# Performance work log

Measured on AMD Instinct MI355X. Metric: run time of the kernel, lower is better.

## Reference

```python
import jax, jax.numpy as jnp
import numpy as np

N_NODES = 65536
N_EDGES = 1048576


def gcn_conv(x, edge_index, edge_weight, W, b):
    """PyG GCNConv: h = D^{-1/2}(A+I)D^{-1/2} x W + b, scatter to target (edge_index[1])."""
    n = x.shape[0]
    row, col = edge_index[0], edge_index[1]
    loop = jnp.arange(n)
    row_f = jnp.concatenate([row, loop])
    col_f = jnp.concatenate([col, loop])
    w_f = jnp.concatenate([edge_weight, jnp.ones((n,), dtype=x.dtype)])
    deg = jax.ops.segment_sum(w_f, col_f, num_segments=n)
    dis = jnp.where(deg > 0, jax.lax.rsqrt(jnp.where(deg > 0, deg, 1.0)), 0.0)
    norm = dis[row_f] * w_f * dis[col_f]  # [E+N]
    h = x @ W  # [N, out]
    msg = h[row_f] * norm[:, None]  # gather + scale
    out = jax.ops.segment_sum(msg, col_f, num_segments=n)
    return out + b


def setup_inputs() -> dict:
    key = jax.random.key(0)
    ks = jax.random.split(key, 8)
    x = jax.random.normal(ks[0], (N_NODES, 128), dtype=jnp.float32)
    edge_index = jax.random.randint(ks[1], (2, N_EDGES), 0, N_NODES, dtype=jnp.int64)
    edge_weight = jax.random.uniform(ks[2], (N_EDGES,), dtype=jnp.float32)
    W1 = jax.random.normal(ks[3], (128, 256), dtype=jnp.float32) * (128 ** -0.5)
    b1 = jnp.zeros((256,), dtype=jnp.float32)
    W2 = jax.random.normal(ks[4], (256, 128), dtype=jnp.float32) * (256 ** -0.5)
    b2 = jnp.zeros((128,), dtype=jnp.float32)
    W3 = jax.random.normal(ks[5], (128, 64), dtype=jnp.float32) * (128 ** -0.5)
    b3 = jnp.zeros((64,), dtype=jnp.float32)
    return {"x": x, "edge_index": edge_index, "edge_weight": edge_weight,
            "num_graphs": 64, "W1": W1, "b1": b1, "W2": W2, "b2": b2, "W3": W3, "b3": b3}


def reference(x, edge_index, edge_weight, num_graphs, W1, b1, W2, b2, W3, b3):
    h = jax.nn.relu(gcn_conv(x, edge_index, edge_weight, W1, b1))
    h = jax.nn.relu(gcn_conv(h, edge_index, edge_weight, W2, b2))
    h = gcn_conv(h, edge_index, edge_weight, W3, b3)  # [N, 64]
    g = h.reshape(num_graphs, -1, 64)
    pad = jnp.zeros((g.shape[0], 1, g.shape[2]), dtype=g.dtype)
    return jnp.concatenate([g, pad], axis=1)  # [num_graphs, nodes_per_graph+1, 64]
```

## Files before the change

### kernel.cpp

```cpp
#include <hip/hip_runtime.h>
#include <cstdint>

#define TPB 256

typedef __attribute__((ext_vector_type(8))) short bf16x8;
typedef __attribute__((ext_vector_type(4))) float f32x4;

__device__ inline unsigned short f2bf(float f) {
  unsigned u = __float_as_uint(f);
  u += 0x7fffu + ((u >> 16) & 1u);
  return (unsigned short)(u >> 16);
}
__device__ inline float bf2f(unsigned short h) {
  return __uint_as_float(((unsigned)h) << 16);
}

__device__ inline void gload_lds16(const void* g, void* l) {
  __builtin_amdgcn_global_load_lds(
      (const __attribute__((address_space(1))) unsigned int*)g,
      (__attribute__((address_space(3))) unsigned int*)l, 16, 0, 0);
}

__device__ inline void acc_bf8(float* acc, int4 raw, float nv) {
  acc[0] += nv * __uint_as_float(((unsigned)raw.x) << 16);
  acc[1] += nv * __uint_as_float(((unsigned)raw.x) & 0xffff0000u);
  acc[2] += nv * __uint_as_float(((unsigned)raw.y) << 16);
  acc[3] += nv * __uint_as_float(((unsigned)raw.y) & 0xffff0000u);
  acc[4] += nv * __uint_as_float(((unsigned)raw.z) << 16);
  acc[5] += nv * __uint_as_float(((unsigned)raw.z) & 0xffff0000u);
  acc[6] += nv * __uint_as_float(((unsigned)raw.w) << 16);
  acc[7] += nv * __uint_as_float(((unsigned)raw.w) & 0xffff0000u);
}


__global__ void k_count_deg(const int* __restrict__ col, const float* __restrict__ w,
                            unsigned long long* __restrict__ pk, int E) {
  int e = blockIdx.x * blockDim.x + threadIdx.x;
  if (e >= E) return;
  int c = col[e];
  unsigned long long inc =
      (1ULL << 40) + (unsigned long long)(unsigned int)(w[e] * 4294967296.0f);
  atomicAdd(&pk[c], inc);
}

__global__ void k_decode(const unsigned long long* __restrict__ pk, float* __restrict__ dis,
                         int* __restrict__ cnt, int n) {
  int i = blockIdx.x * blockDim.x + threadIdx.x;
  if (i >= n) return;
  unsigned long long v = pk[i];
  cnt[i] = (int)(v >> 40);
  float degs = (float)(v & 0xFFFFFFFFFFULL) * 2.3283064365386963e-10f;
  dis[i] = rsqrtf(1.0f + degs);
}


__global__ void k_reduceA(const int* __restrict__ cnt, int* __restrict__ bsum) {
  __shared__ int s[256];
  int t = threadIdx.x;
  s[t] = cnt[blockIdx.x * 256 + t];
  __syncthreads();
  for (int st = 128; st > 0; st >>= 1) {
    if (t < st) s[t] += s[t + st];
    __syncthreads();
  }
  if (t == 0) bsum[blockIdx.x] = s[0];
}

__global__ void k_scanB(const int* __restrict__ bsum, int* __restrict__ boff) {
  __shared__ int s[256];
  int t = threadIdx.x;
  int v = bsum[t];
  s[t] = v;
  __syncthreads();
  for (int st = 1; st < 256; st <<= 1) {
    int a = (t >= st) ? s[t - st] : 0;
    __syncthreads();
    s[t] += a;
    __syncthreads();
  }
  boff[t] = s[t] - v;
}

__global__ void k_scanC(const int* __restrict__ cnt, const int* __restrict__ boff,
                        int* __restrict__ ptr, int* __restrict__ cur, int n) {
  __shared__ int s[256];
  int t = threadIdx.x;
  int i = blockIdx.x * 256 + t;
  int v = cnt[i];
  s[t] = v;
  __syncthreads();
  for (int st = 1; st < 256; st <<= 1) {
    int a = (t >= st) ? s[t - st] : 0;
    __syncthreads();
    s[t] += a;
    __syncthreads();
  }
  int excl = boff[blockIdx.x] + s[t] - v;
  ptr[i] = excl;
  cur[i] = excl;
  if (i == n - 1) ptr[n] = excl + v;
}


__global__ void k_scatter_norm(const int* __restrict__ row, const int* __restrict__ col,
                               const float* __restrict__ w, const float* __restrict__ dis,
                               int* __restrict__ cur, int2* __restrict__ edat, int E) {
  int e = blockIdx.x * blockDim.x + threadIdx.x;
  if (e >= E) return;
  int c = col[e];
  int r = row[e];
  float nv = dis[r] * w[e] * dis[c];
  int p = atomicAdd(&cur[c], 1);
  edat[p] = make_int2(r, __float_as_int(nv));
}


__device__ inline void wprep_one(const float* __restrict__ W, unsigned short* __restrict__ Fh,
                                 unsigned short* __restrict__ Fl, int t, int M) {
  int l = t & 63;
  int rest = t >> 6;
  int nt16 = M >> 4;
  int c0t = rest % nt16;
  int ks = rest / nt16;
  int colg = c0t * 16 + (l & 15);
  int krow = (ks << 5) + ((l >> 4) << 3);
  size_t ob = (size_t)t * 8;
#pragma unroll
  for (int j = 0; j < 8; ++j) {
    float f = W[(size_t)(krow + j) * M + colg];
    unsigned short h = f2bf(f);
    Fh[ob + j] = h;
    Fl[ob + j] = f2bf(f - bf2f(h));
  }
}

__global__ void k_wprep3(const float* __restrict__ W1, const float* __restrict__ W2,
                         const float* __restrict__ W3,
                         unsigned short* __restrict__ f1h, unsigned short* __restrict__ f1l,
                         unsigned short* __restrict__ f2h, unsigned short* __restrict__ f2l,
                         unsigned short* __restrict__ f3h, unsigned short* __restrict__ f3l) {
  int t = blockIdx.x * blockDim.x + threadIdx.x;
  if (t < 4096) wprep_one(W1, f1h, f1l, t, 256);
  else if (t < 8192) wprep_one(W2, f2h, f2l, t - 4096, 128);
  else if (t < 9216) wprep_one(W3, f3h, f3l, t - 8192, 64);
}


template<int GL, bool RELU, bool BIAS, bool SRCBF>
__global__ __launch_bounds__(256) void k_gagg(const int* __restrict__ ptr,
                                              const int2* __restrict__ edat,
                                              const void* __restrict__ srcv,
                                              const float* __restrict__ dis,
                                              const float* __restrict__ bias,
                                              unsigned short* __restrict__ ohi,
                                              unsigned short* __restrict__ olo, int n) {
  constexpr int FPL = SRCBF ? 8 : 4;
  constexpr int F = GL * FPL;
  constexpr int GPB = 256 / GL;
  const int gid = blockIdx.x * GPB + threadIdx.x / GL;
  const int lane = threadIdx.x % GL;
  if (gid >= n) return;
  const int e0 = ptr[gid], e1 = ptr[gid + 1];
  float d = dis[gid];
  float ss = d * d;
  float acc[FPL];
  const float* sF = (const float*)srcv;
  const unsigned short* sB = (const unsigned short*)srcv;
  if constexpr (SRCBF) {
    int4 raw = *reinterpret_cast<const int4*>(sB + (size_t)gid * F + lane * 8);
#pragma unroll
    for (int j = 0; j < 8; ++j) acc[j] = 0.f;
    acc_bf8(acc, raw, ss);
  } else {
    float4 v = *reinterpret_cast<const float4*>(sF + (size_t)gid * F + lane * 4);
    acc[0] = ss * v.x; acc[1] = ss * v.y; acc[2] = ss * v.z; acc[3] = ss * v.w;
  }
  int e = e0;
  for (; e + 8 <= e1; e += 8) {
    int2 ed[8];
#pragma unroll
    for (int u = 0; u < 8; ++u) ed[u] = edat[e + u];
    if constexpr (SRCBF) {
      int4 raw[8];
#pragma unroll
      for (int u = 0; u < 8; ++u)
        raw[u] = *reinterpret_cast<const int4*>(sB + (size_t)ed[u].x * F + lane * 8);
#pragma unroll
      for (int u = 0; u < 8; ++u) acc_bf8(acc, raw[u], __int_as_float(ed[u].y));
    } else {
      float4 v[8];
#pragma unroll
      for (int u = 0; u < 8; ++u)
        v[u] = *reinterpret_cast<const float4*>(sF + (size_t)ed[u].x * F + lane * 4);
#pragma unroll
      for (int u = 0; u < 8; ++u) {
        float nv = __int_as_float(ed[u].y);
        acc[0] += nv * v[u].x; acc[1] += nv * v[u].y;
        acc[2] += nv * v[u].z; acc[3] += nv * v[u].w;
      }
    }
  }
  for (; e + 4 <= e1; e += 4) {
    int2 ed[4];
#pragma unroll
    for (int u = 0; u < 4; ++u) ed[u] = edat[e + u];
    if constexpr (SRCBF) {
      int4 raw[4];
#pragma unroll
      for (int u = 0; u < 4; ++u)
        raw[u] = *reinterpret_cast<const int4*>(sB + (size_t)ed[u].x * F + lane * 8);
#pragma unroll
      for (int u = 0; u < 4; ++u) acc_bf8(acc, raw[u], __int_as_float(ed[u].y));
    } else {
      float4 v[4];
#pragma unroll
      for (int u = 0; u < 4; ++u)
        v[u] = *reinterpret_cast<const float4*>(sF + (size_t)ed[u].x * F + lane * 4);
#pragma unroll
      for (int u = 0; u < 4; ++u) {
        float nv = __int_as_float(ed[u].y);
        acc[0] += nv * v[u].x; acc[1] += nv * v[u].y;
        acc[2] += nv * v[u].z; acc[3] += nv * v[u].w;
      }
    }
  }
  for (; e < e1; ++e) {
    int2 ed = edat[e];
    float nv = __int_as_float(ed.y);
    if constexpr (SRCBF) {
      int4 raw = *reinterpret_cast<const int4*>(sB + (size_t)ed.x * F + lane * 8);
      acc_bf8(acc, raw, nv);
    } else {
      float4 v = *reinterpret_cast<const float4*>(sF + (size_t)ed.x * F + lane * 4);
      acc[0] += nv * v.x; acc[1] += nv * v.y; acc[2] += nv * v.z; acc[3] += nv * v.w;
    }
  }
  if (BIAS) {
#pragma unroll
    for (int j = 0; j < FPL; ++j) acc[j] += bias[lane * FPL + j];
  }
  if (RELU) {
#pragma unroll
    for (int j = 0; j < FPL; ++j) acc[j] = fmaxf(acc[j], 0.f);
  }
  unsigned short hv[FPL], lv[FPL];
#pragma unroll
  for (int j = 0; j < FPL; ++j) {
    hv[j] = f2bf(acc[j]);
    lv[j] = f2bf(acc[j] - bf2f(hv[j]));
  }
  if constexpr (FPL == 4) {
    *reinterpret_cast<ushort4*>(ohi + (size_t)gid * F + lane * 4) = *(ushort4*)hv;
    *reinterpret_cast<ushort4*>(olo + (size_t)gid * F + lane * 4) = *(ushort4*)lv;
  } else {
    *reinterpret_cast<int4*>(ohi + (size_t)gid * F + lane * 8) = *(int4*)hv;
    *reinterpret_cast<int4*>(olo + (size_t)gid * F + lane * 8) = *(int4*)lv;
  }
}

__global__ __launch_bounds__(256) void k_gagg_out(const int* __restrict__ ptr,
                                                  const int2* __restrict__ edat,
                                                  const unsigned short* __restrict__ t3,
                                                  const float* __restrict__ dis,
                                                  const float* __restrict__ b3,
                                                  float* __restrict__ out,
                                                  const int* __restrict__ ngp,
                                                  int n, int nrows) {
  const int gid = blockIdx.x * 32 + threadIdx.x / 8;
  const int lane = threadIdx.x % 8;
  if (gid >= nrows) return;
  const int ng = *ngp;
  const int npg = n / ng;
  const int g = gid / (npg + 1);
  const int r = gid - g * (npg + 1);
  float acc[8] = {0.f, 0.f, 0.f, 0.f, 0.f, 0.f, 0.f, 0.f};
  if (r < npg) {
    const int i = g * npg + r;
    const int e0 = ptr[i], e1 = ptr[i + 1];
    float d = dis[i];
    float ss = d * d;
    int4 sraw = *reinterpret_cast<const int4*>(t3 + (size_t)i * 64 + lane * 8);
    acc_bf8(acc, sraw, ss);
    int e = e0;
    for (; e + 8 <= e1; e += 8) {
      int2 ed[8];
#pragma unroll
      for (int u = 0; u < 8; ++u) ed[u] = edat[e + u];
      int4 raw[8];
#pragma unroll
      for (int u = 0; u < 8; ++u)
        raw[u] = *reinterpret_cast<const int4*>(t3 + (size_t)ed[u].x * 64 + lane * 8);
#pragma unroll
      for (int u = 0; u < 8; ++u) acc_bf8(acc, raw[u], __int_as_float(ed[u].y));
    }
    for (; e + 4 <= e1; e += 4) {
      int2 ed[4];
#pragma unroll
      for (int u = 0; u < 4; ++u) ed[u] = edat[e + u];
      int4 raw[4];
#pragma unroll
      for (int u = 0; u < 4; ++u)
        raw[u] = *reinterpret_cast<const int4*>(t3 + (size_t)ed[u].x * 64 + lane * 8);
#pragma unroll
      for (int u = 0; u < 4; ++u) acc_bf8(acc, raw[u], __int_as_float(ed[u].y));
    }
    for (; e < e1; ++e) {
      int2 ed = edat[e];
      int4 raw = *reinterpret_cast<const int4*>(t3 + (size_t)ed.x * 64 + lane * 8);
      acc_bf8(acc, raw, __int_as_float(ed.y));
    }
#pragma unroll
    for (int j = 0; j < 8; ++j) acc[j] += b3[lane * 8 + j];
  }
  float4 o0 = make_float4(acc[0], acc[1], acc[2], acc[3]);
  float4 o1 = make_float4(acc[4], acc[5], acc[6], acc[7]);
  *reinterpret_cast<float4*>(out + (size_t)gid * 64 + lane * 8) = o0;
  *reinterpret_cast<float4*>(out + (size_t)gid * 64 + lane * 8 + 4) = o1;
}


template<bool BIAS, bool RELU, int OUTM>
__global__ __launch_bounds__(256) void gemm_mfma(
    const unsigned short* __restrict__ Ahi, const unsigned short* __restrict__ Alo,
    const unsigned short* __restrict__ BfHi, const unsigned short* __restrict__ BfLo,
    const float* __restrict__ bias,
    float* __restrict__ Cf, unsigned short* __restrict__ Chi,
    unsigned short* __restrict__ Clo, int K, int M) {
  __shared__ unsigned short AL[2][4096];
  const int tid = threadIdx.x;
  const int l = tid & 63;
  const int w = tid >> 6;
  const int m0 = blockIdx.x * 128;
  const int wmt = (w >> 1) * 4;
  const int wn = (w & 1) * 2;
  const int ntile0 = blockIdx.y * 4 + wn;
  const int nt16 = M >> 4;

  f32x4 acc[4][2];
#pragma unroll
  for (int a = 0; a < 4; ++a)
#pragma unroll
    for (int b = 0; b < 2; ++b) acc[a][b] = f32x4{0.f, 0.f, 0.f, 0.f};

  const int nks = K >> 5;
  for (int ks = 0; ks < nks; ++ks) {
    if (ks) __syncthreads();
#pragma unroll
    for (int rr = 0; rr < 2; ++rr) {
      int s = rr * 256 + tid;
      int mt = s >> 6, sl = s & 63;
      size_t grow = (size_t)(m0 + mt * 16 + (sl & 15)) * K + (ks << 5) + ((sl >> 4) << 3);
      gload_lds16(Ahi + grow, &AL[0][(size_t)s * 8]);
      gload_lds16(Alo + grow, &AL[1][(size_t)s * 8]);
    }
    int4 braw[2][2];
#pragma unroll
    for (int nt = 0; nt < 2; ++nt) {
      size_t bidx = ((size_t)(ks * nt16 + ntile0 + nt) * 64 + l) * 8;
      braw[nt][0] = *reinterpret_cast<const int4*>(BfHi + bidx);
      braw[nt][1] = *reinterpret_cast<const int4*>(BfLo + bidx);
    }
    asm volatile("s_waitcnt vmcnt(0)" ::: "memory");
    __syncthreads();
#pragma unroll
    for (int mt = 0; mt < 4; ++mt) {
      int slot = (wmt + mt) * 64 + l;
      bf16x8 ah = __builtin_bit_cast(bf16x8, *reinterpret_cast<const int4*>(&AL[0][(size_t)slot * 8]));
      bf16x8 al = __builtin_bit_cast(bf16x8, *reinterpret_cast<const int4*>(&AL[1][(size_t)slot * 8]));
#pragma unroll
      for (int nt = 0; nt < 2; ++nt) {
        bf16x8 bh = __builtin_bit_cast(bf16x8, braw[nt][0]);
        bf16x8 bl = __builtin_bit_cast(bf16x8, braw[nt][1]);
        acc[mt][nt] = __builtin_amdgcn_mfma_f32_16x16x32_bf16(al, bh, acc[mt][nt], 0, 0, 0);
        acc[mt][nt] = __builtin_amdgcn_mfma_f32_16x16x32_bf16(ah, bl, acc[mt][nt], 0, 0, 0);
        acc[mt][nt] = __builtin_amdgcn_mfma_f32_16x16x32_bf16(ah, bh, acc[mt][nt], 0, 0, 0);
      }
    }
  }
#pragma unroll
  for (int mt = 0; mt < 4; ++mt) {
    int rowb = m0 + (wmt + mt) * 16 + ((l >> 4) << 2);
#pragma unroll
    for (int nt = 0; nt < 2; ++nt) {
      int colg = (ntile0 + nt) * 16 + (l & 15);
      float bv = 0.f;
      if (BIAS) bv = bias[colg];
#pragma unroll
      for (int i = 0; i < 4; ++i) {
        float v = acc[mt][nt][i] + bv;
        if (RELU) v = fmaxf(v, 0.f);
        size_t off = (size_t)(rowb + i) * M + colg;
        if constexpr (OUTM == 1) {
          unsigned short hh = f2bf(v);
          Chi[off] = hh;
          Clo[off] = f2bf(v - bf2f(hh));
        } else if constexpr (OUTM == 2) {
          Chi[off] = f2bf(v);
        } else {
          Cf[off] = v;
        }
      }
    }
  }
}


static inline int nblk(long work, int tpb = TPB) { return (int)((work + tpb - 1) / tpb); }

extern "C" void kernel_launch(void* const* d_in, const int* in_sizes, int n_in,
                              void* d_out, int out_size, void* d_ws, size_t ws_size,
                              hipStream_t stream) {
  const float* x  = (const float*)d_in[0];
  const int*   ei = (const int*)d_in[1];
  const float* ew = (const float*)d_in[2];
  const int*  ngp = (const int*)d_in[3];
  const float* W1 = (const float*)d_in[4];
  const float* b1 = (const float*)d_in[5];
  const float* W2 = (const float*)d_in[6];
  const float* b2 = (const float*)d_in[7];
  const float* W3 = (const float*)d_in[8];
  const float* b3 = (const float*)d_in[9];
  float* out = (float*)d_out;

  const int n = in_sizes[0] / 128;
  const int E = in_sizes[2];
  const int* row = ei;
  const int* col = ei + E;

  const size_t MB = 1024 * 1024;
  char* W8 = (char*)d_ws;
  int2* edat = (int2*)W8;
  unsigned long long* pk = (unsigned long long*)(W8 + 8 * MB);
  int* cnt   = (int*)(pk + n);
  int* ptrv  = cnt + n;
  int* cur   = ptrv + n + 1;
  int* bsum  = cur + n;
  int* boff  = bsum + 256;
  float* dis = (float*)(boff + 256);
  unsigned short* t1hi = (unsigned short*)(W8 + 16 * MB);
  unsigned short* t1lo = (unsigned short*)(W8 + 32 * MB);
  unsigned short* t2u  = (unsigned short*)(W8 + 16 * MB);
  unsigned short* t3u  = (unsigned short*)(W8 + 16 * MB);
  unsigned short* h1hi = (unsigned short*)(W8 + 56 * MB);
  unsigned short* h1lo = (unsigned short*)(W8 + 88 * MB);
  unsigned short* h2hi = (unsigned short*)(W8 + 56 * MB);
  unsigned short* h2lo = (unsigned short*)(W8 + 72 * MB);
  unsigned short* w1fh = (unsigned short*)(W8 + 120 * MB);
  unsigned short* w1fl = w1fh + 32768;
  unsigned short* w2fh = w1fl + 32768;
  unsigned short* w2fl = w2fh + 32768;
  unsigned short* w3fh = w2fl + 32768;
  unsigned short* w3fl = w3fh + 8192;

  hipMemsetAsync(pk, 0, (size_t)n * 8, stream);
  k_count_deg<<<nblk(E), TPB, 0, stream>>>(col, ew, pk, E);
  k_decode<<<nblk(n), TPB, 0, stream>>>(pk, dis, cnt, n);
  k_reduceA<<<n / 256, 256, 0, stream>>>(cnt, bsum);
  k_scanB<<<1, 256, 0, stream>>>(bsum, boff);
  k_scanC<<<n / 256, 256, 0, stream>>>(cnt, boff, ptrv, cur, n);
  k_scatter_norm<<<nblk(E), TPB, 0, stream>>>(row, col, ew, dis, cur, edat, E);

  k_wprep3<<<nblk(9216), TPB, 0, stream>>>(W1, W2, W3, w1fh, w1fl, w2fh, w2fl, w3fh, w3fl);

  k_gagg<32, false, false, false><<<nblk((long)n * 32), TPB, 0, stream>>>(
      ptrv, edat, x, dis, nullptr, t1hi, t1lo, n);
  {
    dim3 g(n / 128, 256 / 64);
    gemm_mfma<true, true, 1><<<g, 256, 0, stream>>>(
        t1hi, t1lo, w1fh, w1fl, b1, nullptr, h1hi, h1lo, 128, 256);
  }

  {
    dim3 g(n / 128, 128 / 64);
    gemm_mfma<false, false, 2><<<g, 256, 0, stream>>>(
        h1hi, h1lo, w2fh, w2fl, nullptr, nullptr, t2u, nullptr, 256, 128);
  }
  k_gagg<16, true, true, true><<<nblk((long)n * 16), TPB, 0, stream>>>(
      ptrv, edat, t2u, dis, b2, h2hi, h2lo, n);

  {
    dim3 g(n / 128, 64 / 64);
    gemm_mfma<false, false, 2><<<g, 256, 0, stream>>>(
        h2hi, h2lo, w3fh, w3fl, nullptr, nullptr, t3u, nullptr, 128, 64);
  }
  const int nrows = out_size / 64;
  k_gagg_out<<<nblk((long)nrows * 8), TPB, 0, stream>>>(
      ptrv, edat, t3u, dis, b3, out, ngp, n, nrows);
}
```

Baseline: 425.3 us.

## Store activations as single bf16 and spread degree atomics over eight banks

Activations and the input features are now stored as a single bf16 array instead of hi/lo split pairs. This halves gather traffic in the aggregation kernels, drops one MFMA per tile in the GEMMs and removes the second LDS buffer. Separately, the degree-count and CSR-scatter atomics are spread across eight per-block-group copies to cut contention, and a prefix offset per copy is added. The trade-off is lower numeric precision on activations (the weights keep their hi/lo split) plus an extra pass to convert x and compute the per-copy cursors.

```diff
diff --git a/kernel.cpp b/kernel.cpp
--- a/kernel.cpp
+++ b/kernel.cpp
@@ -33,24 +33,46 @@
 }
 
 
-__global__ void k_count_deg(const int* __restrict__ col, const float* __restrict__ w,
-                            unsigned long long* __restrict__ pk, int E) {
+__global__ void k_x2bf(const float* __restrict__ x, unsigned short* __restrict__ xb,
+                       long total8) {
+  long i = blockIdx.x * (long)blockDim.x + threadIdx.x;
+  if (i >= total8) return;
+  const float4* p = reinterpret_cast<const float4*>(x + i * 8);
+  float4 a = p[0], b = p[1];
+  unsigned short h[8];
+  h[0] = f2bf(a.x); h[1] = f2bf(a.y); h[2] = f2bf(a.z); h[3] = f2bf(a.w);
+  h[4] = f2bf(b.x); h[5] = f2bf(b.y); h[6] = f2bf(b.z); h[7] = f2bf(b.w);
+  *reinterpret_cast<int4*>(xb + i * 8) = *(int4*)h;
+}
+
+
+__global__ void k_count_deg8(const int* __restrict__ col, const float* __restrict__ w,
+                             unsigned long long* __restrict__ pk8, int E, int n) {
   int e = blockIdx.x * blockDim.x + threadIdx.x;
   if (e >= E) return;
+  int k = blockIdx.x & 7;
   int c = col[e];
   unsigned long long inc =
       (1ULL << 40) + (unsigned long long)(unsigned int)(w[e] * 4294967296.0f);
-  atomicAdd(&pk[c], inc);
-}
-
-__global__ void k_decode(const unsigned long long* __restrict__ pk, float* __restrict__ dis,
-                         int* __restrict__ cnt, int n) {
+  atomicAdd(&pk8[(size_t)k * n + c], inc);
+}
+
+__global__ void k_decode8(const unsigned long long* __restrict__ pk8,
+                          float* __restrict__ dis, int* __restrict__ cnt,
+                          unsigned short* __restrict__ cum8, int n) {
   int i = blockIdx.x * blockDim.x + threadIdx.x;
   if (i >= n) return;
-  unsigned long long v = pk[i];
-  cnt[i] = (int)(v >> 40);
-  float degs = (float)(v & 0xFFFFFFFFFFULL) * 2.3283064365386963e-10f;
-  dis[i] = rsqrtf(1.0f + degs);
+  unsigned long long tot = 0;
+  int run = 0;
+#pragma unroll
+  for (int k = 0; k < 8; ++k) {
+    unsigned long long v = pk8[(size_t)k * n + i];
+    cum8[(size_t)k * n + i] = (unsigned short)run;
+    run += (int)(v >> 40);
+    tot += v & 0xFFFFFFFFFFULL;
+  }
+  cnt[i] = run;
+  dis[i] = rsqrtf(1.0f + (float)tot * 2.3283064365386963e-10f);
 }
 
 
@@ -82,7 +104,7 @@
 }
 
 __global__ void k_scanC(const int* __restrict__ cnt, const int* __restrict__ boff,
-                        int* __restrict__ ptr, int* __restrict__ cur, int n) {
+                        int* __restrict__ ptr, int n) {
   __shared__ int s[256];
   int t = threadIdx.x;
   int i = blockIdx.x * 256 + t;
@@ -97,20 +119,29 @@
   }
   int excl = boff[blockIdx.x] + s[t] - v;
   ptr[i] = excl;
-  cur[i] = excl;
   if (i == n - 1) ptr[n] = excl + v;
 }
 
-
-__global__ void k_scatter_norm(const int* __restrict__ row, const int* __restrict__ col,
-                               const float* __restrict__ w, const float* __restrict__ dis,
-                               int* __restrict__ cur, int2* __restrict__ edat, int E) {
+__global__ void k_cur8(const int* __restrict__ ptr, const unsigned short* __restrict__ cum8,
+                       int* __restrict__ cur8, int n) {
+  int i = blockIdx.x * blockDim.x + threadIdx.x;
+  if (i >= n) return;
+  int k = blockIdx.y;
+  cur8[(size_t)k * n + i] = ptr[i] + cum8[(size_t)k * n + i];
+}
+
+
+__global__ void k_scatter_norm8(const int* __restrict__ row, const int* __restrict__ col,
+                                const float* __restrict__ w, const float* __restrict__ dis,
+                                int* __restrict__ cur8, int2* __restrict__ edat,
+                                int E, int n) {
   int e = blockIdx.x * blockDim.x + threadIdx.x;
   if (e >= E) return;
+  int k = blockIdx.x & 7;
   int c = col[e];
   int r = row[e];
   float nv = dis[r] * w[e] * dis[c];
-  int p = atomicAdd(&cur[c], 1);
+  int p = atomicAdd(&cur8[(size_t)k * n + c], 1);
   edat[p] = make_int2(r, __float_as_int(nv));
 }
 
@@ -146,16 +177,14 @@
 }
 
 
-template<int GL, bool RELU, bool BIAS, bool SRCBF>
+template<int GL, bool RELU, bool BIAS>
 __global__ __launch_bounds__(256) void k_gagg(const int* __restrict__ ptr,
                                               const int2* __restrict__ edat,
-                                              const void* __restrict__ srcv,
+                                              const unsigned short* __restrict__ src,
                                               const float* __restrict__ dis,
                                               const float* __restrict__ bias,
-                                              unsigned short* __restrict__ ohi,
-                                              unsigned short* __restrict__ olo, int n) {
-  constexpr int FPL = SRCBF ? 8 : 4;
-  constexpr int F = GL * FPL;
+                                              unsigned short* __restrict__ outp, int n) {
+  constexpr int F = GL * 8;
   constexpr int GPB = 256 / GL;
   const int gid = blockIdx.x * GPB + threadIdx.x / GL;
   const int lane = threadIdx.x % GL;
@@ -163,99 +192,51 @@
   const int e0 = ptr[gid], e1 = ptr[gid + 1];
   float d = dis[gid];
   float ss = d * d;
-  float acc[FPL];
-  const float* sF = (const float*)srcv;
-  const unsigned short* sB = (const unsigned short*)srcv;
-  if constexpr (SRCBF) {
-    int4 raw = *reinterpret_cast<const int4*>(sB + (size_t)gid * F + lane * 8);
-#pragma unroll
-    for (int j = 0; j < 8; ++j) acc[j] = 0.f;
+  float acc[8] = {0.f, 0.f, 0.f, 0.f, 0.f, 0.f, 0.f, 0.f};
+  {
+    int4 raw = *reinterpret_cast<const int4*>(src + (size_t)gid * F + lane * 8);
     acc_bf8(acc, raw, ss);
-  } else {
-    float4 v = *reinterpret_cast<const float4*>(sF + (size_t)gid * F + lane * 4);
-    acc[0] = ss * v.x; acc[1] = ss * v.y; acc[2] = ss * v.z; acc[3] = ss * v.w;
   }
   int e = e0;
   for (; e + 8 <= e1; e += 8) {
     int2 ed[8];
 #pragma unroll
     for (int u = 0; u < 8; ++u) ed[u] = edat[e + u];
-    if constexpr (SRCBF) {
-      int4 raw[8];
-#pragma unroll
-      for (int u = 0; u < 8; ++u)
-        raw[u] = *reinterpret_cast<const int4*>(sB + (size_t)ed[u].x * F + lane * 8);
-#pragma unroll
-      for (int u = 0; u < 8; ++u) acc_bf8(acc, raw[u], __int_as_float(ed[u].y));
-    } else {
-      float4 v[8];
-#pragma unroll
-      for (int u = 0; u < 8; ++u)
-        v[u] = *reinterpret_cast<const float4*>(sF + (size_t)ed[u].x * F + lane * 4);
-#pragma unroll
-      for (int u = 0; u < 8; ++u) {
-        float nv = __int_as_float(ed[u].y);
-        acc[0] += nv * v[u].x; acc[1] += nv * v[u].y;
-        acc[2] += nv * v[u].z; acc[3] += nv * v[u].w;
-      }
-    }
+    int4 raw[8];
+#pragma unroll
+    for (int u = 0; u < 8; ++u)
+      raw[u] = *reinterpret_cast<const int4*>(src + (size_t)ed[u].x * F + lane * 8);
+#pragma unroll
+    for (int u = 0; u < 8; ++u) acc_bf8(acc, raw[u], __int_as_float(ed[u].y));
   }
   for (; e + 4 <= e1; e += 4) {
     int2 ed[4];
 #pragma unroll
     for (int u = 0; u < 4; ++u) ed[u] = edat[e + u];
-    if constexpr (SRCBF) {
-      int4 raw[4];
-#pragma unroll
-      for (int u = 0; u < 4; ++u)
-        raw[u] = *reinterpret_cast<const int4*>(sB + (size_t)ed[u].x * F + lane * 8);
-#pragma unroll
-      for (int u = 0; u < 4; ++u) acc_bf8(acc, raw[u], __int_as_float(ed[u].y));
-    } else {
-      float4 v[4];
-#pragma unroll
-      for (int u = 0; u < 4; ++u)
-        v[u] = *reinterpret_cast<const float4*>(sF + (size_t)ed[u].x * F + lane * 4);
-#pragma unroll
-      for (int u = 0; u < 4; ++u) {
-        float nv = __int_as_float(ed[u].y);
-        acc[0] += nv * v[u].x; acc[1] += nv * v[u].y;
-        acc[2] += nv * v[u].z; acc[3] += nv * v[u].w;
-      }
-    }
+    int4 raw[4];
+#pragma unroll
+    for (int u = 0; u < 4; ++u)
+      raw[u] = *reinterpret_cast<const int4*>(src + (size_t)ed[u].x * F + lane * 8);
+#pragma unroll
+    for (int u = 0; u < 4; ++u) acc_bf8(acc, raw[u], __int_as_float(ed[u].y));
   }
   for (; e < e1; ++e) {
     int2 ed = edat[e];
-    float nv = __int_as_float(ed.y);
-    if constexpr (SRCBF) {
-      int4 raw = *reinterpret_cast<const int4*>(sB + (size_t)ed.x * F + lane * 8);
-      acc_bf8(acc, raw, nv);
-    } else {
-      float4 v = *reinterpret_cast<const float4*>(sF + (size_t)ed.x * F + lane * 4);
-      acc[0] += nv * v.x; acc[1] += nv * v.y; acc[2] += nv * v.z; acc[3] += nv * v.w;
-    }
+    int4 raw = *reinterpret_cast<const int4*>(src + (size_t)ed.x * F + lane * 8);
+    acc_bf8(acc, raw, __int_as_float(ed.y));
   }
   if (BIAS) {
 #pragma unroll
-    for (int j = 0; j < FPL; ++j) acc[j] += bias[lane * FPL + j];
+    for (int j = 0; j < 8; ++j) acc[j] += bias[lane * 8 + j];
   }
   if (RELU) {
 #pragma unroll
-    for (int j = 0; j < FPL; ++j) acc[j] = fmaxf(acc[j], 0.f);
-  }
-  unsigned short hv[FPL], lv[FPL];
-#pragma unroll
-  for (int j = 0; j < FPL; ++j) {
-    hv[j] = f2bf(acc[j]);
-    lv[j] = f2bf(acc[j] - bf2f(hv[j]));
-  }
-  if constexpr (FPL == 4) {
-    *reinterpret_cast<ushort4*>(ohi + (size_t)gid * F + lane * 4) = *(ushort4*)hv;
-    *reinterpret_cast<ushort4*>(olo + (size_t)gid * F + lane * 4) = *(ushort4*)lv;
-  } else {
-    *reinterpret_cast<int4*>(ohi + (size_t)gid * F + lane * 8) = *(int4*)hv;
-    *reinterpret_cast<int4*>(olo + (size_t)gid * F + lane * 8) = *(int4*)lv;
-  }
+    for (int j = 0; j < 8; ++j) acc[j] = fmaxf(acc[j], 0.f);
+  }
+  unsigned short hv[8];
+#pragma unroll
+  for (int j = 0; j < 8; ++j) hv[j] = f2bf(acc[j]);
+  *reinterpret_cast<int4*>(outp + (size_t)gid * F + lane * 8) = *(int4*)hv;
 }
 
 __global__ __launch_bounds__(256) void k_gagg_out(const int* __restrict__ ptr,
@@ -319,14 +300,13 @@
 }
 
 
-template<bool BIAS, bool RELU, int OUTM>
+template<bool BIAS, bool RELU>
 __global__ __launch_bounds__(256) void gemm_mfma(
-    const unsigned short* __restrict__ Ahi, const unsigned short* __restrict__ Alo,
+    const unsigned short* __restrict__ A,
     const unsigned short* __restrict__ BfHi, const unsigned short* __restrict__ BfLo,
     const float* __restrict__ bias,
-    float* __restrict__ Cf, unsigned short* __restrict__ Chi,
-    unsigned short* __restrict__ Clo, int K, int M) {
-  __shared__ unsigned short AL[2][4096];
+    unsigned short* __restrict__ C, int K, int M) {
+  __shared__ unsigned short AL[4096];
   const int tid = threadIdx.x;
   const int l = tid & 63;
   const int w = tid >> 6;
@@ -350,8 +330,7 @@
       int s = rr * 256 + tid;
       int mt = s >> 6, sl = s & 63;
       size_t grow = (size_t)(m0 + mt * 16 + (sl & 15)) * K + (ks << 5) + ((sl >> 4) << 3);
-      gload_lds16(Ahi + grow, &AL[0][(size_t)s * 8]);
-      gload_lds16(Alo + grow, &AL[1][(size_t)s * 8]);
+      gload_lds16(A + grow, &AL[(size_t)s * 8]);
     }
     int4 braw[2][2];
 #pragma unroll
@@ -365,15 +344,13 @@
 #pragma unroll
     for (int mt = 0; mt < 4; ++mt) {
       int slot = (wmt + mt) * 64 + l;
-      bf16x8 ah = __builtin_bit_cast(bf16x8, *reinterpret_cast<const int4*>(&AL[0][(size_t)slot * 8]));
-      bf16x8 al = __builtin_bit_cast(bf16x8, *reinterpret_cast<const int4*>(&AL[1][(size_t)slot * 8]));
+      bf16x8 av = __builtin_bit_cast(bf16x8, *reinterpret_cast<const int4*>(&AL[(size_t)slot * 8]));
 #pragma unroll
       for (int nt = 0; nt < 2; ++nt) {
         bf16x8 bh = __builtin_bit_cast(bf16x8, braw[nt][0]);
         bf16x8 bl = __builtin_bit_cast(bf16x8, braw[nt][1]);
-        acc[mt][nt] = __builtin_amdgcn_mfma_f32_16x16x32_bf16(al, bh, acc[mt][nt], 0, 0, 0);
-        acc[mt][nt] = __builtin_amdgcn_mfma_f32_16x16x32_bf16(ah, bl, acc[mt][nt], 0, 0, 0);
-        acc[mt][nt] = __builtin_amdgcn_mfma_f32_16x16x32_bf16(ah, bh, acc[mt][nt], 0, 0, 0);
+        acc[mt][nt] = __builtin_amdgcn_mfma_f32_16x16x32_bf16(av, bl, acc[mt][nt], 0, 0, 0);
+        acc[mt][nt] = __builtin_amdgcn_mfma_f32_16x16x32_bf16(av, bh, acc[mt][nt], 0, 0, 0);
       }
     }
   }
@@ -389,16 +366,7 @@
       for (int i = 0; i < 4; ++i) {
         float v = acc[mt][nt][i] + bv;
         if (RELU) v = fmaxf(v, 0.f);
-        size_t off = (size_t)(rowb + i) * M + colg;
-        if constexpr (OUTM == 1) {
-          unsigned short hh = f2bf(v);
-          Chi[off] = hh;
-          Clo[off] = f2bf(v - bf2f(hh));
-        } else if constexpr (OUTM == 2) {
-          Chi[off] = f2bf(v);
-        } else {
-          Cf[off] = v;
-        }
+        C[(size_t)(rowb + i) * M + colg] = f2bf(v);
       }
     }
   }
@@ -430,58 +398,59 @@
   const size_t MB = 1024 * 1024;
   char* W8 = (char*)d_ws;
   int2* edat = (int2*)W8;
-  unsigned long long* pk = (unsigned long long*)(W8 + 8 * MB);
-  int* cnt   = (int*)(pk + n);
+  unsigned long long* pk8 = (unsigned long long*)(W8 + 8 * MB);
+  int* cnt   = (int*)(W8 + 12 * MB);
   int* ptrv  = cnt + n;
-  int* cur   = ptrv + n + 1;
-  int* bsum  = cur + n;
+  int* bsum  = ptrv + n + 1;
   int* boff  = bsum + 256;
   float* dis = (float*)(boff + 256);
-  unsigned short* t1hi = (unsigned short*)(W8 + 16 * MB);
-  unsigned short* t1lo = (unsigned short*)(W8 + 32 * MB);
-  unsigned short* t2u  = (unsigned short*)(W8 + 16 * MB);
-  unsigned short* t3u  = (unsigned short*)(W8 + 16 * MB);
-  unsigned short* h1hi = (unsigned short*)(W8 + 56 * MB);
-  unsigned short* h1lo = (unsigned short*)(W8 + 88 * MB);
-  unsigned short* h2hi = (unsigned short*)(W8 + 56 * MB);
-  unsigned short* h2lo = (unsigned short*)(W8 + 72 * MB);
-  unsigned short* w1fh = (unsigned short*)(W8 + 120 * MB);
+  unsigned short* cum8 = (unsigned short*)(dis + n);
+  int* cur8  = (int*)(cum8 + 8 * (size_t)n);
+  unsigned short* xb  = (unsigned short*)(W8 + 16 * MB);
+  unsigned short* t1u = (unsigned short*)(W8 + 32 * MB);
+  unsigned short* t2u = (unsigned short*)(W8 + 32 * MB);
+  unsigned short* t3u = (unsigned short*)(W8 + 32 * MB);
+  unsigned short* h1u = (unsigned short*)(W8 + 48 * MB);
+  unsigned short* h2u = (unsigned short*)(W8 + 48 * MB);
+  unsigned short* w1fh = (unsigned short*)(W8 + 80 * MB);
   unsigned short* w1fl = w1fh + 32768;
   unsigned short* w2fh = w1fl + 32768;
   unsigned short* w2fl = w2fh + 32768;
   unsigned short* w3fh = w2fl + 32768;
   unsigned short* w3fl = w3fh + 8192;
 
-  hipMemsetAsync(pk, 0, (size_t)n * 8, stream);
-  k_count_deg<<<nblk(E), TPB, 0, stream>>>(col, ew, pk, E);
-  k_decode<<<nblk(n), TPB, 0, stream>>>(pk, dis, cnt, n);
+  hipMemsetAsync(pk8, 0, (size_t)n * 8 * 8, stream);
+  k_x2bf<<<nblk((long)n * 16), TPB, 0, stream>>>(x, xb, (long)n * 16);
+  k_count_deg8<<<nblk(E), TPB, 0, stream>>>(col, ew, pk8, E, n);
+  k_decode8<<<nblk(n), TPB, 0, stream>>>(pk8, dis, cnt, cum8, n);
   k_reduceA<<<n / 256, 256, 0, stream>>>(cnt, bsum);
   k_scanB<<<1, 256, 0, stream>>>(bsum, boff);
-  k_scanC<<<n / 256, 256, 0, stream>>>(cnt, boff, ptrv, cur, n);
-  k_scatter_norm<<<nblk(E), TPB, 0, stream>>>(row, col, ew, dis, cur, edat, E);
+  k_scanC<<<n / 256, 256, 0, stream>>>(cnt, boff, ptrv, n);
+  {
+    dim3 g(nblk(n), 8);
+    k_cur8<<<g, TPB, 0, stream>>>(ptrv, cum8, cur8, n);
+  }
+  k_scatter_norm8<<<nblk(E), TPB, 0, stream>>>(row, col, ew, dis, cur8, edat, E, n);
 
   k_wprep3<<<nblk(9216), TPB, 0, stream>>>(W1, W2, W3, w1fh, w1fl, w2fh, w2fl, w3fh, w3fl);
 
-  k_gagg<32, false, false, false><<<nblk((long)n * 32), TPB, 0, stream>>>(
-      ptrv, edat, x, dis, nullptr, t1hi, t1lo, n);
+  k_gagg<16, false, false><<<nblk((long)n * 16), TPB, 0, stream>>>(
+      ptrv, edat, xb, dis, nullptr, t1u, n);
   {
     dim3 g(n / 128, 256 / 64);
-    gemm_mfma<true, true, 1><<<g, 256, 0, stream>>>(
-        t1hi, t1lo, w1fh, w1fl, b1, nullptr, h1hi, h1lo, 128, 256);
+    gemm_mfma<true, true><<<g, 256, 0, stream>>>(t1u, w1fh, w1fl, b1, h1u, 128, 256);
   }
 
   {
     dim3 g(n / 128, 128 / 64);
-    gemm_mfma<false, false, 2><<<g, 256, 0, stream>>>(
-        h1hi, h1lo, w2fh, w2fl, nullptr, nullptr, t2u, nullptr, 256, 128);
-  }
-  k_gagg<16, true, true, true><<<nblk((long)n * 16), TPB, 0, stream>>>(
-      ptrv, edat, t2u, dis, b2, h2hi, h2lo, n);
+    gemm_mfma<false, false><<<g, 256, 0, stream>>>(h1u, w2fh, w2fl, nullptr, t2u, 256, 128);
+  }
+  k_gagg<16, true, true><<<nblk((long)n * 16), TPB, 0, stream>>>(
+      ptrv, edat, t2u, dis, b2, h2u, n);
 
   {
     dim3 g(n / 128, 64 / 64);
-    gemm_mfma<false, false, 2><<<g, 256, 0, stream>>>(
-        h2hi, h2lo, w3fh, w3fl, nullptr, nullptr, t3u, nullptr, 128, 64);
+    gemm_mfma<false, false><<<g, 256, 0, stream>>>(h2u, w3fh, w3fl, nullptr, t3u, 128, 64);
   }
   const int nrows = out_size / 64;
   k_gagg_out<<<nblk((long)nrows * 8), TPB, 0, stream>>>(
```

Measured after the change: 373.3 us. -12.2%, faster.
